# Kernel tuning notes

Hardware: AMD Instinct MI355X
Metric: run time of the kernel (lower is better)

The kernel has to match this reference:

```python
import jax, jax.numpy as jnp
import numpy as np

GAMMA = 1.0
MAX_SIMILARITY = 1.0


def setup_inputs() -> dict:
    key = jax.random.key(0)
    k1, k2, k3 = jax.random.split(key, 3)
    B, Ns, D = 64, 1024, 256
    d_vectors = jax.random.normal(k1, (B, Ns, D), dtype=jnp.float32)
    S = jax.random.uniform(k2, (Ns, Ns), dtype=jnp.float32)  # MinMax-normalized sims in [0,1]
    W = (jax.random.uniform(k3, (Ns, Ns)) > 0.3).astype(jnp.float32)  # binary mask (simmat > 0)
    return {"d_vectors": d_vectors, "S": S, "W": W}


def reference(d_vectors, S, W):
    B, Ns, D = d_vectors.shape
    eye = jnp.eye(Ns, dtype=d_vectors.dtype)
    # pairwise L2 distances via ||a-b||^2 = |a|^2 + |b|^2 - 2 a.b  (batched GEMM)
    sq = jnp.sum(d_vectors * d_vectors, axis=-1)                     # [B, Ns]
    G = jnp.einsum('bnd,bmd->bnm', d_vectors, d_vectors)             # [B, Ns, Ns]
    dist2 = jnp.maximum(sq[:, :, None] + sq[:, None, :] - 2.0 * G, 0.0)
    # diagonal of Kd is zeroed below; offset it so sqrt is safe (output unchanged)
    dist = jnp.sqrt(dist2 + eye[None])
    Kd = jnp.exp(-GAMMA * dist)                                      # gram matrix [B, Ns, Ns]
    Kd_tilde = Kd * (1.0 - eye)                                      # Kd - Kd*I
    S_tilde = S - MAX_SIMILARITY * eye                               # [Ns, Ns]
    diff = W[None] * (Kd_tilde - S_tilde[None])
    numer = jnp.sqrt(jnp.sum(diff * diff, axis=(1, 2)))              # per-batch Frobenius norm
    denom = jnp.sqrt(jnp.sum((W - eye) ** 2))
    return jnp.sum(2.0 * numer / denom)
```

## Files before the change

### kernel.cpp

```cpp
#include <hip/hip_runtime.h>
#include <hip/hip_bf16.h>

#define NB 64
#define NS 1024
#define DD 256
#define NT 36
#define THR 120.0f

typedef __attribute__((ext_vector_type(4))) float f32x4;
typedef __attribute__((ext_vector_type(8))) short bf16x8;
typedef __attribute__((ext_vector_type(8))) unsigned short u16x8;
typedef __attribute__((ext_vector_type(4))) unsigned short u16x4;

__device__ __forceinline__ unsigned short f2bf(float x) {
  union { float f; unsigned int u; } c; c.f = x;
  unsigned int r = c.u + 0x7fffu + ((c.u >> 16) & 1u);
  return (unsigned short)(r >> 16);
}


__global__ __launch_bounds__(128) void prep_kernel(const float* __restrict__ din,
                                                   unsigned short* __restrict__ dbf2,
                                                   float* __restrict__ sq,
                                                   int write_bf) {
  __shared__ unsigned short T[16][256];
  const int px = (int)blockIdx.x;
  const int wid = (int)threadIdx.x >> 6;
  const int l = (int)threadIdx.x & 63;
  const int tb = (px & 7) * 512 + (px >> 3);
  const int b = tb >> 6, rt = tb & 63;
  const float4* src =
      reinterpret_cast<const float4*>(din + ((size_t)b * NS + rt * 16) * DD) + l;
  #pragma unroll
  for (int j = 0; j < 8; ++j) {
    const int ri = wid * 8 + j;
    float4 v = src[ri * 64];
    float s = v.x * v.x + v.y * v.y + v.z * v.z + v.w * v.w;
    #pragma unroll
    for (int off = 32; off > 0; off >>= 1) s += __shfl_xor(s, off, 64);
    if (l == 0) sq[(size_t)b * NS + rt * 16 + ri] = s;
    if (write_bf) {
      u16x4 o;
      o[0] = f2bf(v.x); o[1] = f2bf(v.y); o[2] = f2bf(v.z); o[3] = f2bf(v.w);
      const int cp = (l >> 1) ^ (ri & 7);
      *reinterpret_cast<u16x4*>(&T[ri][cp * 8 + (l & 1) * 4]) = o;
    }
  }
  if (!write_bf) return;
  __syncthreads();
  unsigned short* dst = dbf2 + (((size_t)b * 8) * 64 + rt) * 512 + (size_t)l * 8;
  #pragma unroll
  for (int q = 0; q < 4; ++q) {
    const int kg = wid * 4 + q;
    const int cc = (kg * 4 + (l >> 4)) ^ (l & 7);
    u16x8 frag = *reinterpret_cast<const u16x8*>(&T[l & 15][cc * 8]);
    *reinterpret_cast<u16x8*>(dst + (size_t)kg * 64 * 512) = frag;
  }
}

template <int MODE>
__global__ __launch_bounds__(256, 2) void main_kernel(
    const float* __restrict__ dvec, const unsigned short* __restrict__ dbf2,
    const float* __restrict__ sq, const float* __restrict__ S,
    const float* __restrict__ W, float* __restrict__ npart,
    float* __restrict__ dpart, float* __restrict__ cpart) {
  const int tid = threadIdx.x;
  const int lane = tid & 63;
  const int wid = tid >> 6;
  const int orig = (int)blockIdx.x;

  if (orig >= NT * NB) {
    const int blk = orig - NT * NB;
    const int base = blk * 256 + tid;
    float dsum = 0.f, csum = 0.f;
    #pragma unroll
    for (int rpt = 0; rpt < 2; ++rpt) {
      const int idx = base + rpt * 131072;
      float4 w = reinterpret_cast<const float4*>(W)[idx];
      float4 s4 = reinterpret_cast<const float4*>(S)[idx];
      const int e0 = idx << 2;
      const int r = e0 >> 10, c0 = e0 & 1023;
      float wv[4] = {w.x, w.y, w.z, w.w};
      float sv[4] = {s4.x, s4.y, s4.z, s4.w};
      #pragma unroll
      for (int i = 0; i < 4; ++i) {
        const bool dg = (c0 + i) == r;
        const float a = wv[i] - (dg ? 1.0f : 0.0f);
        dsum = fmaf(a, a, dsum);
        const float bq = dg ? (1.0f - sv[i]) : sv[i];
        csum = fmaf(wv[i] * bq, bq, csum);
      }
    }
    #pragma unroll
    for (int off = 32; off > 0; off >>= 1) {
      dsum += __shfl_xor(dsum, off, 64);
      csum += __shfl_xor(csum, off, 64);
    }
    __shared__ float redD[4], redC[4];
    if (lane == 0) { redD[wid] = dsum; redC[wid] = csum; }
    __syncthreads();
    if (tid == 0) {
      dpart[blk] = redD[0] + redD[1] + redD[2] + redD[3];
      cpart[blk] = redC[0] + redC[1] + redC[2] + redC[3];
    }
    return;
  }

  const int wr = wid >> 1;
  const int wc = wid & 1;
  const int bid = (orig & 7) * (NT * NB / 8) + (orig >> 3);
  const int t = bid % NT;
  const int b = bid / NT;
  int u = t, ti = 0;
  while (u >= 8 - ti) { u -= 8 - ti; ++ti; }
  const int tj = ti + u;
  const int brow = ti * 128;
  const int bcol = tj * 128;

  const int rtA0 = ti * 8 + wr * 4;
  const int rtB0 = tj * 8 + wc * 4;

  f32x4 acc[4][4];
  #pragma unroll
  for (int m = 0; m < 4; ++m)
    #pragma unroll
    for (int n = 0; n < 4; ++n) acc[m][n] = f32x4{0.f, 0.f, 0.f, 0.f};

  if (MODE == 0) {
    const unsigned short* pa =
        dbf2 + (((size_t)b * 8) * 64 + rtA0) * 512 + (size_t)lane * 8;
    const unsigned short* pb =
        dbf2 + (((size_t)b * 8) * 64 + rtB0) * 512 + (size_t)lane * 8;
    bf16x8 af[4], bf[4], nf[4];
    #pragma unroll
    for (int m = 0; m < 4; ++m)
      af[m] = *reinterpret_cast<const bf16x8*>(pa + m * 512);
    #pragma unroll
    for (int n = 0; n < 4; ++n)
      bf[n] = *reinterpret_cast<const bf16x8*>(pb + n * 512);
    #pragma unroll
    for (int kg = 0; kg < 8; ++kg) {
      if (kg < 7) {
        #pragma unroll
        for (int m = 0; m < 4; ++m)
          nf[m] = *reinterpret_cast<const bf16x8*>(pa + 32768 + m * 512);
      }
      #pragma unroll
      for (int n = 0; n < 4; ++n) {
        #pragma unroll
        for (int m = 0; m < 4; ++m)
          acc[m][n] = __builtin_amdgcn_mfma_f32_16x16x32_bf16(af[m], bf[n], acc[m][n], 0, 0, 0);
        if (kg < 7)
          bf[n] = *reinterpret_cast<const bf16x8*>(pb + 32768 + n * 512);
      }
      if (kg < 7) {
        #pragma unroll
        for (int m = 0; m < 4; ++m) af[m] = nf[m];
        pa += 32768; pb += 32768;
      }
    }
  } else {
    const float* pbase = dvec + (size_t)b * NS * DD + (lane >> 4) * 8;
    #pragma unroll
    for (int kg = 0; kg < 8; ++kg) {
      bf16x8 af[4], bf[4];
      #pragma unroll
      for (int m = 0; m < 4; ++m) {
        const float* p = pbase + (size_t)((rtA0 + m) * 16 + (lane & 15)) * DD + kg * 32;
        float4 v0 = reinterpret_cast<const float4*>(p)[0];
        float4 v1 = reinterpret_cast<const float4*>(p)[1];
        af[m][0] = (short)f2bf(v0.x); af[m][1] = (short)f2bf(v0.y);
        af[m][2] = (short)f2bf(v0.z); af[m][3] = (short)f2bf(v0.w);
        af[m][4] = (short)f2bf(v1.x); af[m][5] = (short)f2bf(v1.y);
        af[m][6] = (short)f2bf(v1.z); af[m][7] = (short)f2bf(v1.w);
      }
      #pragma unroll
      for (int n = 0; n < 4; ++n) {
        const float* p = pbase + (size_t)((rtB0 + n) * 16 + (lane & 15)) * DD + kg * 32;
        float4 v0 = reinterpret_cast<const float4*>(p)[0];
        float4 v1 = reinterpret_cast<const float4*>(p)[1];
        bf[n][0] = (short)f2bf(v0.x); bf[n][1] = (short)f2bf(v0.y);
        bf[n][2] = (short)f2bf(v0.z); bf[n][3] = (short)f2bf(v0.w);
        bf[n][4] = (short)f2bf(v1.x); bf[n][5] = (short)f2bf(v1.y);
        bf[n][6] = (short)f2bf(v1.z); bf[n][7] = (short)f2bf(v1.w);
      }
      #pragma unroll
      for (int m = 0; m < 4; ++m)
        #pragma unroll
        for (int n = 0; n < 4; ++n)
          acc[m][n] = __builtin_amdgcn_mfma_f32_16x16x32_bf16(af[m], bf[n], acc[m][n], 0, 0, 0);
    }
  }

  const float* sqb = sq + (size_t)b * NS;
  const int hi = lane >> 4, lo = lane & 15;
  float sqc[4];
  #pragma unroll
  for (int n = 0; n < 4; ++n) sqc[n] = sqb[bcol + wc * 64 + n * 16 + lo];
  float dmin = 1e30f;
  #pragma unroll
  for (int m = 0; m < 4; ++m) {
    #pragma unroll
    for (int j = 0; j < 4; ++j) {
      const int r = brow + wr * 64 + m * 16 + hi * 4 + j;
      const float sqr = sqb[r];
      #pragma unroll
      for (int n = 0; n < 4; ++n) {
        const int c = bcol + wc * 64 + n * 16 + lo;
        const float d2 = fmaxf(sqr + sqc[n] - 2.0f * acc[m][n][j], 0.0f);
        dmin = fminf(dmin, (r < c) ? d2 : 1e30f);
      }
    }
  }
  float wsum = 0.f;
  if (__any(dmin < THR)) {
    float lsum = 0.f;
    #pragma unroll
    for (int m = 0; m < 4; ++m) {
      #pragma unroll
      for (int j = 0; j < 4; ++j) {
        const int r = brow + wr * 64 + m * 16 + hi * 4 + j;
        const float sqr = sqb[r];
        #pragma unroll
        for (int n = 0; n < 4; ++n) {
          const int c = bcol + wc * 64 + n * 16 + lo;
          const float d2 = fmaxf(sqr + sqc[n] - 2.0f * acc[m][n][j], 0.0f);
          if ((r < c) && (d2 < THR)) {
            const float kd = __expf(-sqrtf(d2));
            const float wrc = W[(size_t)r * NS + c];
            const float wcr = W[(size_t)c * NS + r];
            const float src_ = S[(size_t)r * NS + c];
            const float scr = S[(size_t)c * NS + r];
            lsum = fmaf(kd, kd * (wrc + wcr) - 2.0f * fmaf(wrc, src_, wcr * scr), lsum);
          }
        }
      }
    }
    #pragma unroll
    for (int off = 32; off > 0; off >>= 1) lsum += __shfl_xor(lsum, off, 64);
    wsum = lsum;
  }
  if (lane == 0) npart[(size_t)bid * 4 + wid] = wsum;
}

__global__ void final_kernel(const float* __restrict__ npart,
                             const float* __restrict__ dpart,
                             const float* __restrict__ cpart,
                             float* __restrict__ out) {
  const int lane = threadIdx.x;
  float dsum = 0.f, csum = 0.f;
  #pragma unroll
  for (int j = 0; j < 8; ++j) {
    dsum += dpart[lane + 64 * j];
    csum += cpart[lane + 64 * j];
  }
  #pragma unroll
  for (int off = 32; off > 0; off >>= 1) {
    dsum += __shfl_xor(dsum, off, 64);
    csum += __shfl_xor(csum, off, 64);
  }
  float nb = 0.f;
  const f32x4* np = reinterpret_cast<const f32x4*>(npart + (size_t)lane * 144);
  #pragma unroll
  for (int j = 0; j < 36; ++j) {
    f32x4 v = np[j];
    nb += v[0] + v[1] + v[2] + v[3];
  }
  float v = 2.0f * sqrtf(csum + nb);
  #pragma unroll
  for (int off = 32; off > 0; off >>= 1) v += __shfl_xor(v, off, 64);
  if (lane == 0) out[0] = v / sqrtf(dsum);
}

extern "C" void kernel_launch(void* const* d_in, const int* in_sizes, int n_in,
                              void* d_out, int out_size, void* d_ws, size_t ws_size,
                              hipStream_t stream) {
  const float* dvec = (const float*)d_in[0];
  const float* S = (const float*)d_in[1];
  const float* W = (const float*)d_in[2];
  float* out = (float*)d_out;

  const size_t bf_bytes = (size_t)NB * NS * DD * sizeof(unsigned short);
  const size_t sq_bytes = (size_t)NB * NS * sizeof(float);
  const size_t small_bytes = sq_bytes + (9216 + 512 + 512) * sizeof(float);
  const bool full = ws_size >= bf_bytes + small_bytes;

  unsigned short* dbf2;
  float* sqp;
  if (full) {
    dbf2 = (unsigned short*)d_ws;
    sqp = (float*)((char*)d_ws + bf_bytes);
  } else {
    dbf2 = nullptr;
    sqp = (float*)d_ws;
  }
  float* npart = sqp + (size_t)NB * NS;
  float* dpart = npart + 9216;
  float* cpart = dpart + 512;

  prep_kernel<<<4096, 128, 0, stream>>>(dvec, dbf2, sqp, full ? 1 : 0);
  if (full)
    main_kernel<0><<<NT * NB + 512, 256, 0, stream>>>(dvec, dbf2, sqp, S, W,
                                                      npart, dpart, cpart);
  else
    main_kernel<1><<<NT * NB + 512, 256, 0, stream>>>(dvec, dbf2, sqp, S, W,
                                                      npart, dpart, cpart);
  final_kernel<<<1, 64, 0, stream>>>(npart, dpart, cpart, out);
}
```

Before: 46.57 us.

## Move W/S reduction into prep kernel and use 2-wave 64x128 warp tiles

The S/W diagonal-norm reduction blocks move from the main GEMM kernel into the prep kernel as 1024 extra 128-thread blocks. The main kernel drops to 128 threads per block, with each wave computing a 64x128 tile (4x8 MFMA fragments) instead of 64x64. This raises B-fragment reuse per wave but doubles the accumulator registers, which can lower occupancy. The partial-sum buffers and final reduction are resized to match.

```diff
diff --git a/kernel.cpp b/kernel.cpp
--- a/kernel.cpp
+++ b/kernel.cpp
@@ -22,92 +22,91 @@
 __global__ __launch_bounds__(128) void prep_kernel(const float* __restrict__ din,
                                                    unsigned short* __restrict__ dbf2,
                                                    float* __restrict__ sq,
+                                                   const float* __restrict__ S,
+                                                   const float* __restrict__ W,
+                                                   float* __restrict__ dpart,
+                                                   float* __restrict__ cpart,
                                                    int write_bf) {
   __shared__ unsigned short T[16][256];
+  __shared__ float redD[2], redC[2];
   const int px = (int)blockIdx.x;
   const int wid = (int)threadIdx.x >> 6;
   const int l = (int)threadIdx.x & 63;
-  const int tb = (px & 7) * 512 + (px >> 3);
-  const int b = tb >> 6, rt = tb & 63;
-  const float4* src =
-      reinterpret_cast<const float4*>(din + ((size_t)b * NS + rt * 16) * DD) + l;
-  #pragma unroll
-  for (int j = 0; j < 8; ++j) {
-    const int ri = wid * 8 + j;
-    float4 v = src[ri * 64];
-    float s = v.x * v.x + v.y * v.y + v.z * v.z + v.w * v.w;
-    #pragma unroll
-    for (int off = 32; off > 0; off >>= 1) s += __shfl_xor(s, off, 64);
-    if (l == 0) sq[(size_t)b * NS + rt * 16 + ri] = s;
-    if (write_bf) {
-      u16x4 o;
-      o[0] = f2bf(v.x); o[1] = f2bf(v.y); o[2] = f2bf(v.z); o[3] = f2bf(v.w);
-      const int cp = (l >> 1) ^ (ri & 7);
-      *reinterpret_cast<u16x4*>(&T[ri][cp * 8 + (l & 1) * 4]) = o;
-    }
-  }
-  if (!write_bf) return;
+  if (px < 4096) {
+    const int tb = (px & 7) * 512 + (px >> 3);
+    const int b = tb >> 6, rt = tb & 63;
+    const float4* src =
+        reinterpret_cast<const float4*>(din + ((size_t)b * NS + rt * 16) * DD) + l;
+    #pragma unroll
+    for (int j = 0; j < 8; ++j) {
+      const int ri = wid * 8 + j;
+      float4 v = src[ri * 64];
+      float s = v.x * v.x + v.y * v.y + v.z * v.z + v.w * v.w;
+      #pragma unroll
+      for (int off = 32; off > 0; off >>= 1) s += __shfl_xor(s, off, 64);
+      if (l == 0) sq[(size_t)b * NS + rt * 16 + ri] = s;
+      if (write_bf) {
+        u16x4 o;
+        o[0] = f2bf(v.x); o[1] = f2bf(v.y); o[2] = f2bf(v.z); o[3] = f2bf(v.w);
+        const int cp = (l >> 1) ^ (ri & 7);
+        *reinterpret_cast<u16x4*>(&T[ri][cp * 8 + (l & 1) * 4]) = o;
+      }
+    }
+    if (!write_bf) return;
+    __syncthreads();
+    unsigned short* dst = dbf2 + (((size_t)b * 8) * 64 + rt) * 512 + (size_t)l * 8;
+    #pragma unroll
+    for (int q = 0; q < 4; ++q) {
+      const int kg = wid * 4 + q;
+      const int cc = (kg * 4 + (l >> 4)) ^ (l & 7);
+      u16x8 frag = *reinterpret_cast<const u16x8*>(&T[l & 15][cc * 8]);
+      *reinterpret_cast<u16x8*>(dst + (size_t)kg * 64 * 512) = frag;
+    }
+    return;
+  }
+  const int blk = px - 4096;
+  float dsum = 0.f, csum = 0.f;
+  #pragma unroll
+  for (int rpt = 0; rpt < 2; ++rpt) {
+    const int idx = blk * 256 + rpt * 128 + (int)threadIdx.x;
+    float4 w = reinterpret_cast<const float4*>(W)[idx];
+    float4 s4 = reinterpret_cast<const float4*>(S)[idx];
+    const int e0 = idx << 2;
+    const int r = e0 >> 10, c0 = e0 & 1023;
+    float wv[4] = {w.x, w.y, w.z, w.w};
+    float sv[4] = {s4.x, s4.y, s4.z, s4.w};
+    #pragma unroll
+    for (int i = 0; i < 4; ++i) {
+      const bool dg = (c0 + i) == r;
+      const float a = wv[i] - (dg ? 1.0f : 0.0f);
+      dsum = fmaf(a, a, dsum);
+      const float bq = dg ? (1.0f - sv[i]) : sv[i];
+      csum = fmaf(wv[i] * bq, bq, csum);
+    }
+  }
+  #pragma unroll
+  for (int off = 32; off > 0; off >>= 1) {
+    dsum += __shfl_xor(dsum, off, 64);
+    csum += __shfl_xor(csum, off, 64);
+  }
+  if (l == 0) { redD[wid] = dsum; redC[wid] = csum; }
   __syncthreads();
-  unsigned short* dst = dbf2 + (((size_t)b * 8) * 64 + rt) * 512 + (size_t)l * 8;
-  #pragma unroll
-  for (int q = 0; q < 4; ++q) {
-    const int kg = wid * 4 + q;
-    const int cc = (kg * 4 + (l >> 4)) ^ (l & 7);
-    u16x8 frag = *reinterpret_cast<const u16x8*>(&T[l & 15][cc * 8]);
-    *reinterpret_cast<u16x8*>(dst + (size_t)kg * 64 * 512) = frag;
+  if (threadIdx.x == 0) {
+    dpart[blk] = redD[0] + redD[1];
+    cpart[blk] = redC[0] + redC[1];
   }
 }
 
 template <int MODE>
-__global__ __launch_bounds__(256, 2) void main_kernel(
+__global__ __launch_bounds__(128, 2) void main_kernel(
     const float* __restrict__ dvec, const unsigned short* __restrict__ dbf2,
-    const float* __restrict__ sq, const float* __restrict__ S,
-    const float* __restrict__ W, float* __restrict__ npart,
-    float* __restrict__ dpart, float* __restrict__ cpart) {
+    const float* __restrict__ sq, float* __restrict__ npart,
+    const float* __restrict__ S, const float* __restrict__ W) {
   const int tid = threadIdx.x;
   const int lane = tid & 63;
   const int wid = tid >> 6;
+
   const int orig = (int)blockIdx.x;
-
-  if (orig >= NT * NB) {
-    const int blk = orig - NT * NB;
-    const int base = blk * 256 + tid;
-    float dsum = 0.f, csum = 0.f;
-    #pragma unroll
-    for (int rpt = 0; rpt < 2; ++rpt) {
-      const int idx = base + rpt * 131072;
-      float4 w = reinterpret_cast<const float4*>(W)[idx];
-      float4 s4 = reinterpret_cast<const float4*>(S)[idx];
-      const int e0 = idx << 2;
-      const int r = e0 >> 10, c0 = e0 & 1023;
-      float wv[4] = {w.x, w.y, w.z, w.w};
-      float sv[4] = {s4.x, s4.y, s4.z, s4.w};
-      #pragma unroll
-      for (int i = 0; i < 4; ++i) {
-        const bool dg = (c0 + i) == r;
-        const float a = wv[i] - (dg ? 1.0f : 0.0f);
-        dsum = fmaf(a, a, dsum);
-        const float bq = dg ? (1.0f - sv[i]) : sv[i];
-        csum = fmaf(wv[i] * bq, bq, csum);
-      }
-    }
-    #pragma unroll
-    for (int off = 32; off > 0; off >>= 1) {
-      dsum += __shfl_xor(dsum, off, 64);
-      csum += __shfl_xor(csum, off, 64);
-    }
-    __shared__ float redD[4], redC[4];
-    if (lane == 0) { redD[wid] = dsum; redC[wid] = csum; }
-    __syncthreads();
-    if (tid == 0) {
-      dpart[blk] = redD[0] + redD[1] + redD[2] + redD[3];
-      cpart[blk] = redC[0] + redC[1] + redC[2] + redC[3];
-    }
-    return;
-  }
-
-  const int wr = wid >> 1;
-  const int wc = wid & 1;
   const int bid = (orig & 7) * (NT * NB / 8) + (orig >> 3);
   const int t = bid % NT;
   const int b = bid / NT;
@@ -117,26 +116,26 @@
   const int brow = ti * 128;
   const int bcol = tj * 128;
 
-  const int rtA0 = ti * 8 + wr * 4;
-  const int rtB0 = tj * 8 + wc * 4;
-
-  f32x4 acc[4][4];
+  const int rtA0 = ti * 8 + wid * 4;
+  const int rtB0 = tj * 8;
+
+  f32x4 acc[4][8];
   #pragma unroll
   for (int m = 0; m < 4; ++m)
     #pragma unroll
-    for (int n = 0; n < 4; ++n) acc[m][n] = f32x4{0.f, 0.f, 0.f, 0.f};
+    for (int n = 0; n < 8; ++n) acc[m][n] = f32x4{0.f, 0.f, 0.f, 0.f};
 
   if (MODE == 0) {
     const unsigned short* pa =
         dbf2 + (((size_t)b * 8) * 64 + rtA0) * 512 + (size_t)lane * 8;
     const unsigned short* pb =
         dbf2 + (((size_t)b * 8) * 64 + rtB0) * 512 + (size_t)lane * 8;
-    bf16x8 af[4], bf[4], nf[4];
+    bf16x8 af[4], bf[8], nf[4];
     #pragma unroll
     for (int m = 0; m < 4; ++m)
       af[m] = *reinterpret_cast<const bf16x8*>(pa + m * 512);
     #pragma unroll
-    for (int n = 0; n < 4; ++n)
+    for (int n = 0; n < 8; ++n)
       bf[n] = *reinterpret_cast<const bf16x8*>(pb + n * 512);
     #pragma unroll
     for (int kg = 0; kg < 8; ++kg) {
@@ -146,7 +145,7 @@
           nf[m] = *reinterpret_cast<const bf16x8*>(pa + 32768 + m * 512);
       }
       #pragma unroll
-      for (int n = 0; n < 4; ++n) {
+      for (int n = 0; n < 8; ++n) {
         #pragma unroll
         for (int m = 0; m < 4; ++m)
           acc[m][n] = __builtin_amdgcn_mfma_f32_16x16x32_bf16(af[m], bf[n], acc[m][n], 0, 0, 0);
@@ -163,7 +162,7 @@
     const float* pbase = dvec + (size_t)b * NS * DD + (lane >> 4) * 8;
     #pragma unroll
     for (int kg = 0; kg < 8; ++kg) {
-      bf16x8 af[4], bf[4];
+      bf16x8 af[4], bf[8];
       #pragma unroll
       for (int m = 0; m < 4; ++m) {
         const float* p = pbase + (size_t)((rtA0 + m) * 16 + (lane & 15)) * DD + kg * 32;
@@ -175,7 +174,7 @@
         af[m][6] = (short)f2bf(v1.z); af[m][7] = (short)f2bf(v1.w);
       }
       #pragma unroll
-      for (int n = 0; n < 4; ++n) {
+      for (int n = 0; n < 8; ++n) {
         const float* p = pbase + (size_t)((rtB0 + n) * 16 + (lane & 15)) * DD + kg * 32;
         float4 v0 = reinterpret_cast<const float4*>(p)[0];
         float4 v1 = reinterpret_cast<const float4*>(p)[1];
@@ -187,26 +186,26 @@
       #pragma unroll
       for (int m = 0; m < 4; ++m)
         #pragma unroll
-        for (int n = 0; n < 4; ++n)
+        for (int n = 0; n < 8; ++n)
           acc[m][n] = __builtin_amdgcn_mfma_f32_16x16x32_bf16(af[m], bf[n], acc[m][n], 0, 0, 0);
     }
   }
 
   const float* sqb = sq + (size_t)b * NS;
   const int hi = lane >> 4, lo = lane & 15;
-  float sqc[4];
-  #pragma unroll
-  for (int n = 0; n < 4; ++n) sqc[n] = sqb[bcol + wc * 64 + n * 16 + lo];
+  float sqc[8];
+  #pragma unroll
+  for (int n = 0; n < 8; ++n) sqc[n] = sqb[bcol + n * 16 + lo];
   float dmin = 1e30f;
   #pragma unroll
   for (int m = 0; m < 4; ++m) {
     #pragma unroll
     for (int j = 0; j < 4; ++j) {
-      const int r = brow + wr * 64 + m * 16 + hi * 4 + j;
+      const int r = brow + wid * 64 + m * 16 + hi * 4 + j;
       const float sqr = sqb[r];
       #pragma unroll
-      for (int n = 0; n < 4; ++n) {
-        const int c = bcol + wc * 64 + n * 16 + lo;
+      for (int n = 0; n < 8; ++n) {
+        const int c = bcol + n * 16 + lo;
         const float d2 = fmaxf(sqr + sqc[n] - 2.0f * acc[m][n][j], 0.0f);
         dmin = fminf(dmin, (r < c) ? d2 : 1e30f);
       }
@@ -219,11 +218,11 @@
     for (int m = 0; m < 4; ++m) {
       #pragma unroll
       for (int j = 0; j < 4; ++j) {
-        const int r = brow + wr * 64 + m * 16 + hi * 4 + j;
+        const int r = brow + wid * 64 + m * 16 + hi * 4 + j;
         const float sqr = sqb[r];
         #pragma unroll
-        for (int n = 0; n < 4; ++n) {
-          const int c = bcol + wc * 64 + n * 16 + lo;
+        for (int n = 0; n < 8; ++n) {
+          const int c = bcol + n * 16 + lo;
           const float d2 = fmaxf(sqr + sqc[n] - 2.0f * acc[m][n][j], 0.0f);
           if ((r < c) && (d2 < THR)) {
             const float kd = __expf(-sqrtf(d2));
@@ -240,7 +239,7 @@
     for (int off = 32; off > 0; off >>= 1) lsum += __shfl_xor(lsum, off, 64);
     wsum = lsum;
   }
-  if (lane == 0) npart[(size_t)bid * 4 + wid] = wsum;
+  if (lane == 0) npart[(size_t)bid * 2 + wid] = wsum;
 }
 
 __global__ void final_kernel(const float* __restrict__ npart,
@@ -250,7 +249,7 @@
   const int lane = threadIdx.x;
   float dsum = 0.f, csum = 0.f;
   #pragma unroll
-  for (int j = 0; j < 8; ++j) {
+  for (int j = 0; j < 16; ++j) {
     dsum += dpart[lane + 64 * j];
     csum += cpart[lane + 64 * j];
   }
@@ -260,9 +259,9 @@
     csum += __shfl_xor(csum, off, 64);
   }
   float nb = 0.f;
-  const f32x4* np = reinterpret_cast<const f32x4*>(npart + (size_t)lane * 144);
-  #pragma unroll
-  for (int j = 0; j < 36; ++j) {
+  const f32x4* np = reinterpret_cast<const f32x4*>(npart + (size_t)lane * 72);
+  #pragma unroll
+  for (int j = 0; j < 18; ++j) {
     f32x4 v = np[j];
     nb += v[0] + v[1] + v[2] + v[3];
   }
@@ -282,7 +281,7 @@
 
   const size_t bf_bytes = (size_t)NB * NS * DD * sizeof(unsigned short);
   const size_t sq_bytes = (size_t)NB * NS * sizeof(float);
-  const size_t small_bytes = sq_bytes + (9216 + 512 + 512) * sizeof(float);
+  const size_t small_bytes = sq_bytes + (4608 + 1024 + 1024) * sizeof(float);
   const bool full = ws_size >= bf_bytes + small_bytes;
 
   unsigned short* dbf2;
@@ -295,15 +294,14 @@
     sqp = (float*)d_ws;
   }
   float* npart = sqp + (size_t)NB * NS;
-  float* dpart = npart + 9216;
-  float* cpart = dpart + 512;
-
-  prep_kernel<<<4096, 128, 0, stream>>>(dvec, dbf2, sqp, full ? 1 : 0);
+  float* dpart = npart + 4608;
+  float* cpart = dpart + 1024;
+
+  prep_kernel<<<4096 + 1024, 128, 0, stream>>>(dvec, dbf2, sqp, S, W,
+                                               dpart, cpart, full ? 1 : 0);
   if (full)
-    main_kernel<0><<<NT * NB + 512, 256, 0, stream>>>(dvec, dbf2, sqp, S, W,
-                                                      npart, dpart, cpart);
+    main_kernel<0><<<NT * NB, 128, 0, stream>>>(dvec, dbf2, sqp, npart, S, W);
   else
-    main_kernel<1><<<NT * NB + 512, 256, 0, stream>>>(dvec, dbf2, sqp, S, W,
-                                                      npart, dpart, cpart);
+    main_kernel<1><<<NT * NB, 128, 0, stream>>>(dvec, dbf2, sqp, npart, S, W);
   final_kernel<<<1, 64, 0, stream>>>(npart, dpart, cpart, out);
 }
```

Result: slower. 57.26 us (+22.9%).
